# Performance work log

Hardware: AMD Instinct MI355X
Metric: run time of the kernel (lower is better)

## Reference

```python
import jax, jax.numpy as jnp
import numpy as np

NB, NC = 100000, 10000   # buildings, communities
EB, EC = 400000, 80000   # edges
BD, CD = 64, 32          # feature dims


def _glorot(key, shape):
    fan_in = shape[-2] if len(shape) > 1 else shape[0]
    return jax.random.normal(key, shape, jnp.float32) * (1.0 / np.sqrt(fan_in))


def setup_inputs() -> dict:
    key = jax.random.key(0)
    ks = iter(jax.random.split(key, 40))
    inp = {}
    inp['building_features'] = jax.random.normal(next(ks), (NB, BD), jnp.float32)
    inp['community_features'] = jax.random.normal(next(ks), (NC, CD), jnp.float32)
    inp['building_edge_index'] = jax.random.randint(next(ks), (2, EB), 0, NB, jnp.int32)
    inp['community_edge_index'] = jax.random.randint(next(ks), (2, EC), 0, NC, jnp.int32)
    inp['building_to_comm_mapping'] = jax.random.randint(next(ks), (NB,), 0, NC, jnp.int32)
    inp['c1_wl'] = _glorot(next(ks), (CD, 512)); inp['c1_wr'] = _glorot(next(ks), (CD, 512))
    inp['c1_att'] = _glorot(next(ks), (8, 64)); inp['c1_b'] = jnp.zeros((512,), jnp.float32)
    inp['c2_wl'] = _glorot(next(ks), (512, 128)); inp['c2_wr'] = _glorot(next(ks), (512, 128))
    inp['c2_att'] = _glorot(next(ks), (4, 32)); inp['c2_b'] = jnp.zeros((128,), jnp.float32)
    # feature attention: 8 heads of MLP (64+128)->128->2
    inp['fa_w1'] = _glorot(next(ks), (8, BD + 128, 128)); inp['fa_b1'] = jnp.zeros((8, 128), jnp.float32)
    inp['fa_w2'] = _glorot(next(ks), (8, 128, 2)); inp['fa_b2'] = jnp.zeros((8, 2), jnp.float32)
    inp['b1_wl'] = _glorot(next(ks), (BD + 128, 512)); inp['b1_wr'] = _glorot(next(ks), (BD + 128, 512))
    inp['b1_att'] = _glorot(next(ks), (8, 64)); inp['b1_b'] = jnp.zeros((512,), jnp.float32)
    inp['b2_wl'] = _glorot(next(ks), (512, 128)); inp['b2_wr'] = _glorot(next(ks), (512, 128))
    inp['b2_att'] = _glorot(next(ks), (4, 32)); inp['b2_b'] = jnp.zeros((128,), jnp.float32)
    inp['b3_wl'] = _glorot(next(ks), (128, 2)); inp['b3_wr'] = _glorot(next(ks), (128, 2))
    inp['b3_att'] = _glorot(next(ks), (1, 2)); inp['b3_b'] = jnp.zeros((2,), jnp.float32)
    return inp


def gatv2(x, src, dst, wl, wr, att, b, heads, out_dim, concat=True):
    """PyG GATv2Conv (eval mode, self-loops already appended to src/dst)."""
    n = x.shape[0]
    xl = (x @ wl).reshape(n, heads, out_dim)  # source transform
    xr = (x @ wr).reshape(n, heads, out_dim)  # target transform
    e = jax.nn.leaky_relu(xl[src] + xr[dst], 0.2)          # [E,H,D]
    logits = jnp.einsum('ehd,hd->eh', e, att)              # [E,H]
    m = jax.ops.segment_max(logits, dst, num_segments=n)   # stable softmax per target
    p = jnp.exp(logits - m[dst])
    denom = jax.ops.segment_sum(p, dst, num_segments=n)
    alpha = p / denom[dst]
    agg = jax.ops.segment_sum(alpha[:, :, None] * xl[src], dst, num_segments=n)
    agg = agg.reshape(n, heads * out_dim) if concat else agg.mean(axis=1)
    return agg + b


def _with_self_loops(edge_index, n):
    loops = jnp.arange(n, dtype=edge_index.dtype)
    return (jnp.concatenate([edge_index[0], loops]), jnp.concatenate([edge_index[1], loops]))


def _forward(building_features, community_features,
             c1_wl, c1_wr, c1_att, c1_b, c2_wl, c2_wr, c2_att, c2_b,
             fa_w1, fa_b1, fa_w2, fa_b2,
             b1_wl, b1_wr, b1_att, b1_b, b2_wl, b2_wr, b2_att, b2_b,
             b3_wl, b3_wr, b3_att, b3_b,
             building_edge_index, community_edge_index, building_to_comm_mapping):
    csrc, cdst = _with_self_loops(community_edge_index, NC)
    bsrc, bdst = _with_self_loops(building_edge_index, NB)
    # community GNN (dropout is identity in eval)
    cx = jax.nn.relu(gatv2(community_features, csrc, cdst, c1_wl, c1_wr, c1_att, c1_b, 8, 64))
    cx = jax.nn.relu(gatv2(cx, csrc, cdst, c2_wl, c2_wr, c2_att, c2_b, 4, 32))  # [NC,128]
    bcf = cx[building_to_comm_mapping]                                          # [NB,128]
    # multi-head feature attention fusion (vectorized over 8 heads)
    combined = jnp.concatenate([building_features, bcf], axis=1)                # [NB,192]
    h = jax.nn.relu(jnp.einsum('nf,hfk->nhk', combined, fa_w1) + fa_b1)         # [NB,8,128]
    w = jax.nn.softmax(jnp.einsum('nhk,hko->nho', h, fa_w2) + fa_b2, axis=-1)   # [NB,8,2]
    wmean = w.mean(axis=1)                                                      # mean over heads == mean of weighted copies
    fused = jnp.concatenate([building_features * wmean[:, 0:1], bcf * wmean[:, 1:2]], axis=1)
    # building GNN (single batched graph == Batch.from_data_list over all communities)
    x = jax.nn.relu(gatv2(fused, bsrc, bdst, b1_wl, b1_wr, b1_att, b1_b, 8, 64))
    x = jax.nn.relu(gatv2(x, bsrc, bdst, b2_wl, b2_wr, b2_att, b2_b, 4, 32))
    x = gatv2(x, bsrc, bdst, b3_wl, b3_wr, b3_att, b3_b, 1, 2)                   # [NB,2]
    return jax.nn.log_softmax(x, axis=1)


def reference(building_features, community_features,
              c1_wl, c1_wr, c1_att, c1_b, c2_wl, c2_wr, c2_att, c2_b,
              fa_w1, fa_b1, fa_w2, fa_b2,
              b1_wl, b1_wr, b1_att, b1_b, b2_wl, b2_wr, b2_att, b2_b,
              b3_wl, b3_wr, b3_att, b3_b,
              building_edge_index, community_edge_index, building_to_comm_mapping):
    return _forward(building_features, community_features,
                    c1_wl, c1_wr, c1_att, c1_b, c2_wl, c2_wr, c2_att, c2_b,
                    fa_w1, fa_b1, fa_w2, fa_b2,
                    b1_wl, b1_wr, b1_att, b1_b, b2_wl, b2_wr, b2_att, b2_b,
                    b3_wl, b3_wr, b3_att, b3_b,
                    building_edge_index, community_edge_index, building_to_comm_mapping)
```

## Files before the change

kernel.cpp:

```cpp
#include <hip/hip_runtime.h>

static constexpr int NBLD = 100000, NCOM = 10000, EBU = 400000, ECO = 80000;
static constexpr int EBT = EBU + NBLD;
static constexpr int ECT = ECO + NCOM;

typedef _Float16 f16;
typedef _Float16 f16x2 __attribute__((ext_vector_type(2)));
typedef _Float16 f16x8 __attribute__((ext_vector_type(8)));
typedef float f32x4 __attribute__((ext_vector_type(4)));

static constexpr size_t OFF_X1H  = 0;
static constexpr size_t OFF_CXL  = 0;
static constexpr size_t OFF_CXR  = 10240000;
static constexpr size_t OFF_CX1  = 20480000;
static constexpr size_t OFF_CX2L = 30720000;
static constexpr size_t OFF_CX2R = 33280000;
static constexpr size_t OFF_X2   = 0;
static constexpr size_t OFF_XLH  = 102400000;
static constexpr size_t OFF_XRH  = 128000000;
static constexpr size_t OFF_XL2  = 102400000;
static constexpr size_t OFF_XR2  = 128000000;
static constexpr size_t OFF_BF16 = 153600000;
static constexpr size_t OFF_CXF16= 166400000;
static constexpr size_t OFF_WM   = 168960000;
static constexpr size_t OFF_XL3  = 169760000;
static constexpr size_t OFF_XR3  = 170560000;
static constexpr size_t OFF_FAW  = 171360000;
static constexpr size_t OFF_B1LT = 171753216;
static constexpr size_t OFF_B1RT = 171949824;
static constexpr size_t OFF_B2T  = 172146432;
static constexpr size_t OFF_BOFF = 172408576;
static constexpr size_t OFF_BCUR = 172808592;
static constexpr size_t OFF_BSRC = 173208592;
static constexpr size_t OFF_COFF = 175208592;
static constexpr size_t OFF_CCUR = 175248608;
static constexpr size_t OFF_CSRC = 175288608;
static constexpr size_t OFF_SC1  = 175648608;
static constexpr size_t OFF_SC2  = 175649632;
static constexpr size_t OFF_SC1C = 175650656;
static constexpr size_t OFF_SC2C = 175651680;
static constexpr size_t OFF_C1T  = 175700000;
static constexpr size_t OFF_C2T  = 175765536;
static constexpr size_t OFF_CF16 = 176027680;

static constexpr int LP = 40;

__global__ void k_zerof(float* __restrict__ p, int n) {
  int i = blockIdx.x * blockDim.x + threadIdx.x;
  if (i < n) p[i] = 0.f;
}

__global__ void k_cvt4(const float* __restrict__ a, f16* __restrict__ b, int n4) {
  int i = blockIdx.x * blockDim.x + threadIdx.x;
  if (i >= n4) return;
  float4 f = *(const float4*)(a + (size_t)i * 4);
  f16x2 h0; h0[0] = (f16)f.x; h0[1] = (f16)f.y;
  f16x2 h1; h1[0] = (f16)f.z; h1[1] = (f16)f.w;
  *(unsigned*)(b + (size_t)i * 4)     = __builtin_bit_cast(unsigned, h0);
  *(unsigned*)(b + (size_t)i * 4 + 2) = __builtin_bit_cast(unsigned, h1);
}

__global__ void k_cvtall(const float* __restrict__ fa_w1,
                         const float* __restrict__ b1_wl, const float* __restrict__ b1_wr,
                         const float* __restrict__ b2_wl, const float* __restrict__ b2_wr,
                         const float* __restrict__ c1_wl, const float* __restrict__ c1_wr,
                         const float* __restrict__ c2_wl, const float* __restrict__ c2_wr,
                         f16* __restrict__ FAW, f16* __restrict__ B1LT, f16* __restrict__ B1RT,
                         f16* __restrict__ B2T, f16* __restrict__ C1T, f16* __restrict__ C2T) {
  int seg = blockIdx.y;
  const float* W; f16* T; int K, N;
  if (seg < 8)        { W = fa_w1 + (size_t)seg * 192 * 128; T = FAW + (size_t)seg * 128 * 192; K = 192; N = 128; }
  else if (seg == 8)  { W = b1_wl; T = B1LT; K = 192; N = 512; }
  else if (seg == 9)  { W = b1_wr; T = B1RT; K = 192; N = 512; }
  else if (seg == 10) { W = b2_wl; T = B2T;  K = 512; N = 128; }
  else if (seg == 11) { W = b2_wr; T = B2T + 128 * 512; K = 512; N = 128; }
  else if (seg == 12) { W = c1_wl; T = C1T;  K = 32;  N = 512; }
  else if (seg == 13) { W = c1_wr; T = C1T + 512 * 32; K = 32; N = 512; }
  else if (seg == 14) { W = c2_wl; T = C2T;  K = 512; N = 128; }
  else                { W = c2_wr; T = C2T + 128 * 512; K = 512; N = 128; }
  int i = blockIdx.x * blockDim.x + threadIdx.x;
  if (i >= K * N) return;
  int n = i / K, k = i - n * K;
  T[(size_t)n * K + k] = (f16)W[(size_t)k * N + n];
}

__global__ void k_zero2(int* __restrict__ a, int na, int* __restrict__ b, int nb) {
  int i = blockIdx.x * blockDim.x + threadIdx.x;
  if (i < na) a[i] = 0;
  else if (i - na < nb) b[i - na] = 0;
}

__global__ void k_count2(const int* __restrict__ bdst, const int* __restrict__ cdst,
                         int* __restrict__ bcnt, int* __restrict__ ccnt) {
  int e = blockIdx.x * blockDim.x + threadIdx.x;
  if (e < EBT) {
    int dst = (e < EBU) ? bdst[e] : (e - EBU);
    atomicAdd(&bcnt[dst], 1);
  } else {
    int e2 = e - EBT;
    if (e2 >= ECT) return;
    int dst = (e2 < ECO) ? cdst[e2] : (e2 - ECO);
    atomicAdd(&ccnt[dst], 1);
  }
}

__global__ void k_scan1g(const int* __restrict__ bcnt, const int* __restrict__ ccnt,
                         int* __restrict__ boff, int* __restrict__ coff,
                         int* __restrict__ bsum, int* __restrict__ csum) {
  const int* cnt = blockIdx.y ? ccnt : bcnt;
  int* off = blockIdx.y ? coff : boff;
  int* sum = blockIdx.y ? csum : bsum;
  int N = blockIdx.y ? NCOM : NBLD;
  __shared__ int sh[256];
  int tid = threadIdx.x;
  int base = blockIdx.x * 2048 + tid * 8;
  int c[8]; int s = 0;
#pragma unroll
  for (int j = 0; j < 8; ++j) { int i = base + j; c[j] = (i < N) ? cnt[i] : 0; s += c[j]; }
  sh[tid] = s; __syncthreads();
  int own = s;
  for (int o = 1; o < 256; o <<= 1) {
    int v = (tid >= o) ? sh[tid - o] : 0; __syncthreads();
    sh[tid] += v; __syncthreads();
  }
  int ex = sh[tid] - own;
#pragma unroll
  for (int j = 0; j < 8; ++j) { int i = base + j; if (i < N) off[i] = ex; ex += c[j]; }
  if (tid == 255) sum[blockIdx.x] = sh[255];
}

__global__ void k_scan2g(const int* __restrict__ bsum, const int* __restrict__ csum,
                         int nb, int nc, int* __restrict__ bpre, int* __restrict__ cpre) {
  const int* sum = blockIdx.x ? csum : bsum;
  int n = blockIdx.x ? nc : nb;
  int* pre = blockIdx.x ? cpre : bpre;
  __shared__ int sh[256];
  int tid = threadIdx.x;
  int v0 = (tid < n) ? sum[tid] : 0;
  sh[tid] = v0; __syncthreads();
  for (int o = 1; o < 256; o <<= 1) {
    int v = (tid >= o) ? sh[tid - o] : 0; __syncthreads();
    sh[tid] += v; __syncthreads();
  }
  pre[tid] = sh[tid] - v0;
}

__global__ void k_scan3c(int* __restrict__ off, int N, const int* __restrict__ bpre, int Et,
                         int* __restrict__ cur) {
  int i = blockIdx.x * blockDim.x + threadIdx.x;
  if (i < N) {
    int v = off[i] + bpre[i >> 11];
    off[i] = v;
    cur[i] = v;
  }
  if (i == 0) off[N] = Et;
}

__global__ void k_scatter2(const int* __restrict__ bsrc, const int* __restrict__ bdst,
                           const int* __restrict__ csrc, const int* __restrict__ cdst,
                           int* __restrict__ bcur, int* __restrict__ ccur,
                           int* __restrict__ bout, int* __restrict__ cout) {
  int e = blockIdx.x * blockDim.x + threadIdx.x;
  if (e < EBT) {
    int s, d;
    if (e < EBU) { s = bsrc[e]; d = bdst[e]; } else { s = d = e - EBU; }
    bout[atomicAdd(&bcur[d], 1)] = s;
  } else {
    int e2 = e - EBT;
    if (e2 >= ECT) return;
    int s, d;
    if (e2 < ECO) { s = csrc[e2]; d = cdst[e2]; } else { s = d = e2 - ECO; }
    cout[atomicAdd(&ccur[d], 1)] = s;
  }
}


struct frag32 { f16x8 v0, v1; };

static __device__ inline frag32 loadA_lin(const f16* __restrict__ X, int lda,
                                          int k0, int tid, int bm, int M) {
  int row = tid >> 1, half = tid & 1;
  int grow = bm + row;
  frag32 r; r.v0 = (f16x8){}; r.v1 = (f16x8){};
  if (grow < M) {
    const f16* p = X + (size_t)grow * lda + k0 + half * 16;
    r.v0 = *(const f16x8*)(p);
    r.v1 = *(const f16x8*)(p + 8);
  }
  return r;
}

template<bool SCALE>
static __device__ inline frag32 loadA_fused(const f16* __restrict__ bf16h,
                                            const f16* __restrict__ cx16, int mrow,
                                            f16 s0, f16 s1, int k0, int tid, int grow, int M) {
  int half = tid & 1;
  int gc = k0 + half * 16;
  frag32 r; r.v0 = (f16x8){}; r.v1 = (f16x8){};
  if (grow < M) {
    const f16* src; f16 s;
    if (gc < 64) { src = bf16h + (size_t)grow * 64 + gc; s = s0; }
    else         { src = cx16 + (size_t)mrow * 128 + (gc - 64); s = s1; }
    r.v0 = *(const f16x8*)(src);
    r.v1 = *(const f16x8*)(src + 8);
    if (SCALE) {
#pragma unroll
      for (int j = 0; j < 8; ++j) { r.v0[j] *= s; r.v1[j] *= s; }
    }
  }
  return r;
}

static __device__ inline frag32 loadB_T(const f16* __restrict__ WT, int ldk, int k0, int tid) {
  int col = tid >> 1, half = tid & 1;
  const f16* p = WT + (size_t)col * ldk + k0 + half * 16;
  frag32 r;
  r.v0 = *(const f16x8*)(p);
  r.v1 = *(const f16x8*)(p + 8);
  return r;
}

static __device__ inline frag32 loadB_Tpair(const f16* __restrict__ WLt, const f16* __restrict__ WRt,
                                            int ldk, int slab, int k0, int tid) {
  int col = tid >> 1, half = tid & 1;
  const f16* base = (col < 64) ? (WLt + (size_t)(slab + col) * ldk)
                               : (WRt + (size_t)(slab + col - 64) * ldk);
  const f16* p = base + k0 + half * 16;
  frag32 r;
  r.v0 = *(const f16x8*)(p);
  r.v1 = *(const f16x8*)(p + 8);
  return r;
}

static __device__ inline void writeFrag(f16 (*S)[LP], frag32 f, int tid) {
  int row = tid >> 1, half = tid & 1;
  *(f16x8*)&S[row][half * 16]     = f.v0;
  *(f16x8*)&S[row][half * 16 + 8] = f.v1;
}

static __device__ inline void mma_tiles(const f16 (*As)[LP], const f16 (*Bs)[LP],
                                        f32x4 acc[4][4], int wm, int wn, int lane) {
  int rl = lane & 15;
  int kg = (lane >> 4) * 8;
  f16x8 a[4], b[4];
#pragma unroll
  for (int i = 0; i < 4; ++i) a[i] = *(const f16x8*)&As[wm * 64 + i * 16 + rl][kg];
#pragma unroll
  for (int j = 0; j < 4; ++j) b[j] = *(const f16x8*)&Bs[wn * 64 + j * 16 + rl][kg];
#pragma unroll
  for (int i = 0; i < 4; ++i)
#pragma unroll
    for (int j = 0; j < 4; ++j)
      acc[i][j] = __builtin_amdgcn_mfma_f32_16x16x32_f16(a[i], b[j], acc[i][j], 0, 0, 0);
}

template<int NCB>
__global__ __launch_bounds__(256) void k_mgemm_gen(
    const f16* __restrict__ A, int lda,
    const f16* __restrict__ WT, int K,
    f16* __restrict__ out0, f16* __restrict__ out1, int N0, int ldo, int M) {
  __shared__ f16 As[2][128][LP];
  __shared__ f16 Bs[2][128][LP];
  int tid = threadIdx.x;
  int ppx = gridDim.x / (8 * NCB);
  int xcd = blockIdx.x & 7;
  int j6 = blockIdx.x >> 3;
  int cb = j6 % NCB;
  int p = xcd * ppx + j6 / NCB;
  int bm = p * 128;
  if (bm >= M) return;
  int bn = cb * 128;
  int lane = tid & 63, w = tid >> 6, wm_ = w >> 1, wn = w & 1;
  f32x4 acc[4][4];
#pragma unroll
  for (int i = 0; i < 4; ++i)
#pragma unroll
    for (int j = 0; j < 4; ++j) acc[i][j] = (f32x4){0.f, 0.f, 0.f, 0.f};

  const f16* WTb = WT + (size_t)bn * K;
  int NT = K >> 5;
  frag32 a0 = loadA_lin(A, lda, 0, tid, bm, M);
  frag32 b0 = loadB_T(WTb, K, 0, tid);
  frag32 a1; a1.v0 = (f16x8){}; a1.v1 = (f16x8){};
  frag32 b1v = a1;
  if (NT > 1) { a1 = loadA_lin(A, lda, 32, tid, bm, M); b1v = loadB_T(WTb, K, 32, tid); }
  for (int t = 0; t < NT; t += 2) {
    writeFrag(As[0], a0, tid); writeFrag(Bs[0], b0, tid);
    bool two = (t + 1 < NT);
    if (two) { writeFrag(As[1], a1, tid); writeFrag(Bs[1], b1v, tid); }
    __syncthreads();
    if (t + 2 < NT) {
      a0 = loadA_lin(A, lda, (t + 2) * 32, tid, bm, M);
      b0 = loadB_T(WTb, K, (t + 2) * 32, tid);
      if (t + 3 < NT) {
        a1 = loadA_lin(A, lda, (t + 3) * 32, tid, bm, M);
        b1v = loadB_T(WTb, K, (t + 3) * 32, tid);
      }
    }
    mma_tiles(As[0], Bs[0], acc, wm_, wn, lane);
    if (two) mma_tiles(As[1], Bs[1], acc, wm_, wn, lane);
    __syncthreads();
  }
  int rbase = bm + wm_ * 64 + (lane >> 4) * 4;
  int cl = lane & 15;
#pragma unroll
  for (int mi = 0; mi < 4; ++mi)
#pragma unroll
    for (int ni = 0; ni < 4; ++ni) {
      int col = bn + wn * 64 + ni * 16 + cl;
      f16* o; int c;
      if (col < N0) { o = out0; c = col; } else { o = out1; c = col - N0; }
#pragma unroll
      for (int r = 0; r < 4; ++r) {
        int row = rbase + mi * 16 + r;
        if (row < M) o[(size_t)row * ldo + c] = (f16)acc[mi][ni][r];
      }
    }
}

__global__ __launch_bounds__(256) void k_mgemm_b1(
    const f16* __restrict__ bf16h, const f16* __restrict__ cx16,
    const int* __restrict__ map, const float* __restrict__ wmv,
    const f16* __restrict__ WLt, const f16* __restrict__ WRt, int slabBase,
    f16* __restrict__ outl, f16* __restrict__ outr, int M) {
  __shared__ f16 As[2][128][LP];
  __shared__ f16 Bs[2][128][LP];
  int tid = threadIdx.x;
  int ppx = gridDim.x >> 4;
  int xcd = blockIdx.x & 7;
  int j6 = blockIdx.x >> 3;
  int ch = j6 & 1;
  int p = xcd * ppx + (j6 >> 1);
  int bm = p * 128;
  if (bm >= M) return;
  int slab = slabBase + ch * 64;
  int colbase = ch * 64;
  int lane = tid & 63, w = tid >> 6, wm_ = w >> 1, wn = w & 1;
  f32x4 acc[4][4];
#pragma unroll
  for (int i = 0; i < 4; ++i)
#pragma unroll
    for (int j = 0; j < 4; ++j) acc[i][j] = (f32x4){0.f, 0.f, 0.f, 0.f};

  int arow = bm + (tid >> 1);
  int mrow = 0; f16 s0 = (f16)1.f, s1 = (f16)1.f;
  if (arow < M) {
    mrow = map[arow];
    s0 = (f16)wmv[(size_t)arow * 2];
    s1 = (f16)wmv[(size_t)arow * 2 + 1];
  }

  frag32 a0 = loadA_fused<true>(bf16h, cx16, mrow, s0, s1, 0, tid, arow, M);
  frag32 b0 = loadB_Tpair(WLt, WRt, 192, slab, 0, tid);
  frag32 a1 = loadA_fused<true>(bf16h, cx16, mrow, s0, s1, 32, tid, arow, M);
  frag32 b1v = loadB_Tpair(WLt, WRt, 192, slab, 32, tid);
  for (int t = 0; t < 6; t += 2) {
    writeFrag(As[0], a0, tid); writeFrag(Bs[0], b0, tid);
    writeFrag(As[1], a1, tid); writeFrag(Bs[1], b1v, tid);
    __syncthreads();
    if (t + 2 < 6) {
      a0 = loadA_fused<true>(bf16h, cx16, mrow, s0, s1, (t + 2) * 32, tid, arow, M);
      b0 = loadB_Tpair(WLt, WRt, 192, slab, (t + 2) * 32, tid);
      a1 = loadA_fused<true>(bf16h, cx16, mrow, s0, s1, (t + 3) * 32, tid, arow, M);
      b1v = loadB_Tpair(WLt, WRt, 192, slab, (t + 3) * 32, tid);
    }
    mma_tiles(As[0], Bs[0], acc, wm_, wn, lane);
    mma_tiles(As[1], Bs[1], acc, wm_, wn, lane);
    __syncthreads();
  }
  int rbase = bm + wm_ * 64 + (lane >> 4) * 4;
  int cl = lane & 15;
#pragma unroll
  for (int mi = 0; mi < 4; ++mi)
#pragma unroll
    for (int ni = 0; ni < 4; ++ni) {
      int col = wn * 64 + ni * 16 + cl;
      f16* o = (col < 64) ? outl : outr;
      int c = colbase + (col & 63);
#pragma unroll
      for (int r = 0; r < 4; ++r) {
        int row = rbase + mi * 16 + r;
        if (row < M) o[(size_t)row * 128 + c] = (f16)acc[mi][ni][r];
      }
    }
}

__global__ __launch_bounds__(256) void k_mgemm_fa(
    const f16* __restrict__ bf16h, const f16* __restrict__ cx16,
    const int* __restrict__ map,
    const f16* __restrict__ w1T, const float* __restrict__ b1,
    const float* __restrict__ w2, const float* __restrict__ b2,
    float* __restrict__ wmout, int M) {
  __shared__ f16 As[2][128][LP];
  __shared__ f16 Bs[2][128][LP];
  __shared__ float sred[128][4];
  int tid = threadIdx.x;
  int ppx = gridDim.x >> 6;
  int xcd = blockIdx.x & 7;
  int j6 = blockIdx.x >> 3;
  int p = xcd * ppx + (j6 >> 3);
  int h = j6 & 7;
  int bm = p * 128;
  if (bm >= M) return;
  int lane = tid & 63, w = tid >> 6, wm_ = w >> 1, wn = w & 1;
  f32x4 acc[4][4];
#pragma unroll
  for (int i = 0; i < 4; ++i)
#pragma unroll
    for (int j = 0; j < 4; ++j) acc[i][j] = (f32x4){0.f, 0.f, 0.f, 0.f};

  int arow = bm + (tid >> 1);
  int mrow = (arow < M) ? map[arow] : 0;
  const f16* WT = w1T + (size_t)h * 128 * 192;

  frag32 a0 = loadA_fused<false>(bf16h, cx16, mrow, (f16)1.f, (f16)1.f, 0, tid, arow, M);
  frag32 b0 = loadB_T(WT, 192, 0, tid);
  frag32 a1 = loadA_fused<false>(bf16h, cx16, mrow, (f16)1.f, (f16)1.f, 32, tid, arow, M);
  frag32 b1v = loadB_T(WT, 192, 32, tid);
  for (int t = 0; t < 6; t += 2) {
    writeFrag(As[0], a0, tid); writeFrag(Bs[0], b0, tid);
    writeFrag(As[1], a1, tid); writeFrag(Bs[1], b1v, tid);
    __syncthreads();
    if (t + 2 < 6) {
      a0 = loadA_fused<false>(bf16h, cx16, mrow, (f16)1.f, (f16)1.f, (t + 2) * 32, tid, arow, M);
      b0 = loadB_T(WT, 192, (t + 2) * 32, tid);
      a1 = loadA_fused<false>(bf16h, cx16, mrow, (f16)1.f, (f16)1.f, (t + 3) * 32, tid, arow, M);
      b1v = loadB_T(WT, 192, (t + 3) * 32, tid);
    }
    mma_tiles(As[0], Bs[0], acc, wm_, wn, lane);
    mma_tiles(As[1], Bs[1], acc, wm_, wn, lane);
    __syncthreads();
  }

  int cl = lane & 15;
#pragma unroll
  for (int mi = 0; mi < 4; ++mi) {
    float t0[4] = {0.f, 0.f, 0.f, 0.f}, t1[4] = {0.f, 0.f, 0.f, 0.f};
#pragma unroll
    for (int ni = 0; ni < 4; ++ni) {
      int col = wn * 64 + ni * 16 + cl;
      float b1c = b1[h * 128 + col];
      float w0c = w2[((size_t)h * 128 + col) * 2];
      float w1c = w2[((size_t)h * 128 + col) * 2 + 1];
#pragma unroll
      for (int r = 0; r < 4; ++r) {
        float hv = fmaxf(acc[mi][ni][r] + b1c, 0.f);
        t0[r] = fmaf(hv, w0c, t0[r]);
        t1[r] = fmaf(hv, w1c, t1[r]);
      }
    }
#pragma unroll
    for (int m = 1; m < 16; m <<= 1) {
#pragma unroll
      for (int r = 0; r < 4; ++r) { t0[r] += __shfl_xor(t0[r], m); t1[r] += __shfl_xor(t1[r], m); }
    }
    if (cl == 0) {
#pragma unroll
      for (int r = 0; r < 4; ++r) {
        int rib = wm_ * 64 + mi * 16 + (lane >> 4) * 4 + r;
        sred[rib][wn] = t0[r];
        sred[rib][2 + wn] = t1[r];
      }
    }
  }
  __syncthreads();
  if (tid < 128) {
    int grow = bm + tid;
    if (grow < M) {
      float l0 = sred[tid][0] + sred[tid][1] + b2[h * 2];
      float l1 = sred[tid][2] + sred[tid][3] + b2[h * 2 + 1];
      float mx = fmaxf(l0, l1);
      float e0 = __expf(l0 - mx), e1 = __expf(l1 - mx);
      float inv = 0.125f / (e0 + e1);
      atomicAdd(&wmout[(size_t)grow * 2], e0 * inv);
      atomicAdd(&wmout[(size_t)grow * 2 + 1], e1 * inv);
    }
  }
}

template<int V, int G, bool RELU, typename IT, typename OT>
__global__ __launch_bounds__(256) void k_convf(const IT* __restrict__ xl, const IT* __restrict__ xr,
                                               const float* __restrict__ attw, const float* __restrict__ bias,
                                               const int* __restrict__ off, const int* __restrict__ srcl,
                                               OT* __restrict__ outp, int N, int ldx, int ldo) {
  int n = (int)((blockIdx.x * (unsigned)blockDim.x + threadIdx.x) >> 6);
  if (n >= N) return;
  int lane = threadIdx.x & 63;
  int base = lane * V;
  float xr_r[V], att_r[V], acc[V];
#pragma unroll
  for (int j = 0; j < V; ++j) {
    xr_r[j] = (float)xr[(size_t)n * ldx + base + j];
    att_r[j] = attw[base + j];
    acc[j] = 0.f;
  }
  float mh = -INFINITY, lh = 0.f;
  int p0 = off[n], p1 = off[n + 1];

  f16 rawn[V];
  auto ldrow = [&](int src, f16* dst) {
    if constexpr (V == 2 && sizeof(IT) == 2) {
      *(f16x2*)dst = *(const f16x2*)(&xl[(size_t)src * ldx + base]);
    } else if constexpr (V == 8 && sizeof(IT) == 2) {
      *(f16x8*)dst = *(const f16x8*)(&xl[(size_t)src * ldx + base]);
    } else {
#pragma unroll
      for (int j = 0; j < V; ++j) dst[j] = (f16)xl[(size_t)src * ldx + base + j];
    }
  };
  if (p0 < p1) ldrow(srcl[p0], rawn);
  for (int p = p0; p < p1; ++p) {
    f16 raw[V];
#pragma unroll
    for (int j = 0; j < V; ++j) raw[j] = rawn[j];
    if (p + 1 < p1) ldrow(srcl[p + 1], rawn);
    float xlv[V];
#pragma unroll
    for (int j = 0; j < V; ++j) xlv[j] = (float)raw[j];
    float part = 0.f;
#pragma unroll
    for (int j = 0; j < V; ++j) {
      float t = xlv[j] + xr_r[j];
      t = t > 0.f ? t : 0.2f * t;
      part = fmaf(t, att_r[j], part);
    }
#pragma unroll
    for (int m = 1; m < G; m <<= 1) part += __shfl_xor(part, m);
    float mn = fmaxf(mh, part);
    float scl = __expf(mh - mn);
    float pe = __expf(part - mn);
    lh = lh * scl + pe;
#pragma unroll
    for (int j = 0; j < V; ++j) acc[j] = acc[j] * scl + pe * xlv[j];
    mh = mn;
  }
  float inv = 1.f / lh;
#pragma unroll
  for (int j = 0; j < V; ++j) {
    float v = fmaf(acc[j], inv, bias[base + j]);
    if (RELU) v = fmaxf(v, 0.f);
    outp[(size_t)n * ldo + base + j] = (OT)v;
  }
}

__global__ __launch_bounds__(256) void k_b3gemm(const float* __restrict__ x2, const float* __restrict__ wl,
                                                const float* __restrict__ wr,
                                                float* __restrict__ xl3, float* __restrict__ xr3, int NB) {
  int n = (int)((blockIdx.x * (unsigned)blockDim.x + threadIdx.x) >> 6);
  if (n >= NB) return;
  int lane = threadIdx.x & 63;
  float2 a = *(const float2*)(x2 + (size_t)n * 128 + lane * 2);
  float4 wlv = *(const float4*)(wl + lane * 4);
  float4 wrv = *(const float4*)(wr + lane * 4);
  float l0 = a.x * wlv.x + a.y * wlv.z;
  float l1 = a.x * wlv.y + a.y * wlv.w;
  float r0 = a.x * wrv.x + a.y * wrv.z;
  float r1 = a.x * wrv.y + a.y * wrv.w;
#pragma unroll
  for (int m = 1; m < 64; m <<= 1) {
    l0 += __shfl_xor(l0, m); l1 += __shfl_xor(l1, m);
    r0 += __shfl_xor(r0, m); r1 += __shfl_xor(r1, m);
  }
  if (lane == 0) {
    xl3[(size_t)n * 2] = l0; xl3[(size_t)n * 2 + 1] = l1;
    xr3[(size_t)n * 2] = r0; xr3[(size_t)n * 2 + 1] = r1;
  }
}

__global__ void k_conv3(const float* __restrict__ xl, const float* __restrict__ xr,
                        const float* __restrict__ att, const float* __restrict__ bias,
                        const int* __restrict__ off, const int* __restrict__ srcl,
                        float* __restrict__ out, int NB) {
  int n = blockIdx.x * blockDim.x + threadIdx.x;
  if (n >= NB) return;
  float a0 = att[0], a1 = att[1];
  float xr0 = xr[(size_t)n * 2], xr1 = xr[(size_t)n * 2 + 1];
  float mh = -INFINITY, lh = 0.f, c0 = 0.f, c1 = 0.f;
  int p0 = off[n], p1 = off[n + 1];
  float2 rawn = make_float2(0.f, 0.f);
  if (p0 < p1) rawn = *(const float2*)(xl + (size_t)srcl[p0] * 2);
  for (int p = p0; p < p1; ++p) {
    float sl0 = rawn.x, sl1 = rawn.y;
    if (p + 1 < p1) rawn = *(const float2*)(xl + (size_t)srcl[p + 1] * 2);
    float t0 = sl0 + xr0; t0 = t0 > 0.f ? t0 : 0.2f * t0;
    float t1 = sl1 + xr1; t1 = t1 > 0.f ? t1 : 0.2f * t1;
    float lg = t0 * a0 + t1 * a1;
    float mn = fmaxf(mh, lg);
    float scl = __expf(mh - mn);
    float pe = __expf(lg - mn);
    lh = lh * scl + pe;
    c0 = c0 * scl + pe * sl0;
    c1 = c1 * scl + pe * sl1;
    mh = mn;
  }
  float inv = 1.f / lh;
  float v0 = c0 * inv + bias[0];
  float v1 = c1 * inv + bias[1];
  float mx = fmaxf(v0, v1);
  float ls = mx + logf(__expf(v0 - mx) + __expf(v1 - mx));
  out[(size_t)n * 2] = v0 - ls;
  out[(size_t)n * 2 + 1] = v1 - ls;
}

static inline int cdiv(int a, int b) { return (a + b - 1) / b; }

extern "C" void kernel_launch(void* const* d_in, const int* in_sizes, int n_in,
                              void* d_out, int out_size, void* d_ws, size_t ws_size,
                              hipStream_t stream) {
  (void)in_sizes; (void)n_in; (void)out_size; (void)ws_size;
  const float* bfeat = (const float*)d_in[0];
  const float* cfeat = (const float*)d_in[1];
  const int* bei = (const int*)d_in[2];
  const int* cei = (const int*)d_in[3];
  const int* b2c = (const int*)d_in[4];
  const float* c1_wl = (const float*)d_in[5];
  const float* c1_wr = (const float*)d_in[6];
  const float* c1_att = (const float*)d_in[7];
  const float* c1_b = (const float*)d_in[8];
  const float* c2_wl = (const float*)d_in[9];
  const float* c2_wr = (const float*)d_in[10];
  const float* c2_att = (const float*)d_in[11];
  const float* c2_b = (const float*)d_in[12];
  const float* fa_w1 = (const float*)d_in[13];
  const float* fa_b1 = (const float*)d_in[14];
  const float* fa_w2 = (const float*)d_in[15];
  const float* fa_b2 = (const float*)d_in[16];
  const float* b1_wl = (const float*)d_in[17];
  const float* b1_wr = (const float*)d_in[18];
  const float* b1_att = (const float*)d_in[19];
  const float* b1_b = (const float*)d_in[20];
  const float* b2_wl = (const float*)d_in[21];
  const float* b2_wr = (const float*)d_in[22];
  const float* b2_att = (const float*)d_in[23];
  const float* b2_b = (const float*)d_in[24];
  const float* b3_wl = (const float*)d_in[25];
  const float* b3_wr = (const float*)d_in[26];
  const float* b3_att = (const float*)d_in[27];
  const float* b3_b = (const float*)d_in[28];
  char* ws = (char*)d_ws;
  float* out = (float*)d_out;

  const int* b_src_arr = bei;
  const int* b_dst_arr = bei + EBU;
  const int* c_src_arr = cei;
  const int* c_dst_arr = cei + ECO;

  f16*   X1H  = (f16*)(ws + OFF_X1H);
  float* X2   = (float*)(ws + OFF_X2);
  f16*   XLH  = (f16*)(ws + OFF_XLH);
  f16*   XRH  = (f16*)(ws + OFF_XRH);
  f16*   XL2  = (f16*)(ws + OFF_XL2);
  f16*   XR2  = (f16*)(ws + OFF_XR2);
  f16*   CXLh = (f16*)(ws + OFF_CXL);
  f16*   CXRh = (f16*)(ws + OFF_CXR);
  f16*   CX1h = (f16*)(ws + OFF_CX1);
  f16*   CX2Lh= (f16*)(ws + OFF_CX2L);
  f16*   CX2Rh= (f16*)(ws + OFF_CX2R);
  f16*   BF16 = (f16*)(ws + OFF_BF16);
  f16*   CXF16= (f16*)(ws + OFF_CXF16);
  float* WM   = (float*)(ws + OFF_WM);
  float* XL3  = (float*)(ws + OFF_XL3);
  float* XR3  = (float*)(ws + OFF_XR3);
  f16*   FAW  = (f16*)(ws + OFF_FAW);
  f16*   B1LT = (f16*)(ws + OFF_B1LT);
  f16*   B1RT = (f16*)(ws + OFF_B1RT);
  f16*   B2T  = (f16*)(ws + OFF_B2T);
  f16*   C1T  = (f16*)(ws + OFF_C1T);
  f16*   C2T  = (f16*)(ws + OFF_C2T);
  f16*   CF16 = (f16*)(ws + OFF_CF16);
  int* BOFF = (int*)(ws + OFF_BOFF);
  int* BCUR = (int*)(ws + OFF_BCUR);
  int* BSRC = (int*)(ws + OFF_BSRC);
  int* COFF = (int*)(ws + OFF_COFF);
  int* CCUR = (int*)(ws + OFF_CCUR);
  int* CSRC = (int*)(ws + OFF_CSRC);
  int* SC1  = (int*)(ws + OFF_SC1);
  int* SC2  = (int*)(ws + OFF_SC2);
  int* SC1C = (int*)(ws + OFF_SC1C);
  int* SC2C = (int*)(ws + OFF_SC2C);

  k_cvtall<<<dim3(cdiv(192 * 512, 256), 16), 256, 0, stream>>>(
      fa_w1, b1_wl, b1_wr, b2_wl, b2_wr, c1_wl, c1_wr, c2_wl, c2_wr,
      FAW, B1LT, B1RT, B2T, C1T, C2T);
  k_cvt4<<<cdiv(NBLD * 16, 256), 256, 0, stream>>>(bfeat, BF16, NBLD * 16);
  k_cvt4<<<cdiv(NCOM * 8, 256), 256, 0, stream>>>(cfeat, CF16, NCOM * 8);

  k_zero2<<<cdiv(NBLD + NCOM, 256), 256, 0, stream>>>(BCUR, NBLD, CCUR, NCOM);
  k_count2<<<cdiv(EBT + ECT, 256), 256, 0, stream>>>(b_dst_arr, c_dst_arr, BCUR, CCUR);
  k_scan1g<<<dim3(cdiv(NBLD, 2048), 2), 256, 0, stream>>>(BCUR, CCUR, BOFF, COFF, SC1, SC1C);
  k_scan2g<<<2, 256, 0, stream>>>(SC1, SC1C, cdiv(NBLD, 2048), cdiv(NCOM, 2048), SC2, SC2C);
  k_scan3c<<<cdiv(NBLD, 256), 256, 0, stream>>>(BOFF, NBLD, SC2, EBT, BCUR);
  k_scan3c<<<cdiv(NCOM, 256), 256, 0, stream>>>(COFF, NCOM, SC2C, ECT, CCUR);
  k_scatter2<<<cdiv(EBT + ECT, 256), 256, 0, stream>>>(
      b_src_arr, b_dst_arr, c_src_arr, c_dst_arr, BCUR, CCUR, BSRC, CSRC);

  {
    int pC = cdiv(cdiv(NCOM, 128), 8);
    k_mgemm_gen<8><<<8 * pC * 8, 256, 0, stream>>>(
        CF16, 32, C1T, 32, CXLh, CXRh, 512, 512, NCOM);
    k_convf<8, 8, true, f16, f16><<<cdiv(NCOM, 4), 256, 0, stream>>>(
        CXLh, CXRh, c1_att, c1_b, COFF, CSRC, CX1h, NCOM, 512, 512);
    k_mgemm_gen<2><<<8 * pC * 2, 256, 0, stream>>>(
        CX1h, 512, C2T, 512, CX2Lh, CX2Rh, 128, 128, NCOM);
    k_convf<2, 16, true, f16, f16><<<cdiv(NCOM, 4), 256, 0, stream>>>(
        CX2Lh, CX2Rh, c2_att, c2_b, COFF, CSRC, CXF16, NCOM, 128, 128);
  }

  k_zerof<<<cdiv(NBLD * 2, 256), 256, 0, stream>>>(WM, NBLD * 2);
  {
    int panels = cdiv(NBLD, 128);
    int ppx = cdiv(panels, 8);
    k_mgemm_fa<<<64 * ppx, 256, 0, stream>>>(
        BF16, CXF16, b2c, FAW, fa_b1, fa_w2, fa_b2, WM, NBLD);
  }

  {
    int pB = cdiv(cdiv(NBLD, 128), 8);
    for (int cp = 0; cp < 4; ++cp) {
      k_mgemm_b1<<<16 * pB, 256, 0, stream>>>(
          BF16, CXF16, b2c, WM, B1LT, B1RT, cp * 128, XLH, XRH, NBLD);
      k_convf<2, 32, true, f16, f16><<<cdiv(NBLD, 4), 256, 0, stream>>>(
          XLH, XRH, b1_att + cp * 128, b1_b + cp * 128, BOFF, BSRC, X1H + cp * 128, NBLD, 128, 512);
    }
    k_mgemm_gen<2><<<8 * pB * 2, 256, 0, stream>>>(
        X1H, 512, B2T, 512, XL2, XR2, 128, 128, NBLD);
  }

  k_convf<2, 16, true, f16, float><<<cdiv(NBLD, 4), 256, 0, stream>>>(
      XL2, XR2, b2_att, b2_b, BOFF, BSRC, X2, NBLD, 128, 128);

  k_b3gemm<<<cdiv(NBLD, 4), 256, 0, stream>>>(X2, b3_wl, b3_wr, XL3, XR3, NBLD);
  k_conv3<<<cdiv(NBLD, 256), 256, 0, stream>>>(XL3, XR3, b3_att, b3_b, BOFF, BSRC, out, NBLD);
}
```

Baseline: 931.3 us.

## Deepen GEMM register prefetch to four stages with one barrier per k-step

The three MFMA GEMM kernels (generic, b1, fa) now keep four k-tiles of A and B in registers instead of two. The main loop handles one k-tile per iteration, ping-ponging between the two LDS buffers, so it needs one __syncthreads per tile instead of two per pair of tiles. The generic GEMM also takes K as a template parameter, so its loop fully unrolls with constant trip counts. The aim is to hide more global-load latency and cut barrier overhead, at the cost of more VGPRs, which may lower occupancy.

Result: no change. 944.7 us (+1.4%).

```diff
diff --git a/kernel.cpp b/kernel.cpp
--- a/kernel.cpp
+++ b/kernel.cpp
@@ -254,11 +254,12 @@
       acc[i][j] = __builtin_amdgcn_mfma_f32_16x16x32_f16(a[i], b[j], acc[i][j], 0, 0, 0);
 }
 
-template<int NCB>
+template<int K, int NCB>
 __global__ __launch_bounds__(256) void k_mgemm_gen(
     const f16* __restrict__ A, int lda,
-    const f16* __restrict__ WT, int K,
+    const f16* __restrict__ WT,
     f16* __restrict__ out0, f16* __restrict__ out1, int N0, int ldo, int M) {
+  constexpr int NT = K >> 5;
   __shared__ f16 As[2][128][LP];
   __shared__ f16 Bs[2][128][LP];
   int tid = threadIdx.x;
@@ -278,29 +279,22 @@
     for (int j = 0; j < 4; ++j) acc[i][j] = (f32x4){0.f, 0.f, 0.f, 0.f};
 
   const f16* WTb = WT + (size_t)bn * K;
-  int NT = K >> 5;
-  frag32 a0 = loadA_lin(A, lda, 0, tid, bm, M);
-  frag32 b0 = loadB_T(WTb, K, 0, tid);
-  frag32 a1; a1.v0 = (f16x8){}; a1.v1 = (f16x8){};
-  frag32 b1v = a1;
-  if (NT > 1) { a1 = loadA_lin(A, lda, 32, tid, bm, M); b1v = loadB_T(WTb, K, 32, tid); }
-  for (int t = 0; t < NT; t += 2) {
-    writeFrag(As[0], a0, tid); writeFrag(Bs[0], b0, tid);
-    bool two = (t + 1 < NT);
-    if (two) { writeFrag(As[1], a1, tid); writeFrag(Bs[1], b1v, tid); }
+  frag32 ra[4], rb[4];
+#pragma unroll
+  for (int t = 0; t < 4; ++t)
+    if (t < NT) { ra[t] = loadA_lin(A, lda, t * 32, tid, bm, M); rb[t] = loadB_T(WTb, K, t * 32, tid); }
+#pragma unroll
+  for (int t = 0; t < NT; ++t) {
+    writeFrag(As[t & 1], ra[t & 3], tid);
+    writeFrag(Bs[t & 1], rb[t & 3], tid);
     __syncthreads();
-    if (t + 2 < NT) {
-      a0 = loadA_lin(A, lda, (t + 2) * 32, tid, bm, M);
-      b0 = loadB_T(WTb, K, (t + 2) * 32, tid);
-      if (t + 3 < NT) {
-        a1 = loadA_lin(A, lda, (t + 3) * 32, tid, bm, M);
-        b1v = loadB_T(WTb, K, (t + 3) * 32, tid);
-      }
-    }
-    mma_tiles(As[0], Bs[0], acc, wm_, wn, lane);
-    if (two) mma_tiles(As[1], Bs[1], acc, wm_, wn, lane);
-    __syncthreads();
-  }
+    if (t + 4 < NT) {
+      ra[t & 3] = loadA_lin(A, lda, (t + 4) * 32, tid, bm, M);
+      rb[t & 3] = loadB_T(WTb, K, (t + 4) * 32, tid);
+    }
+    mma_tiles(As[t & 1], Bs[t & 1], acc, wm_, wn, lane);
+  }
+  __syncthreads();
   int rbase = bm + wm_ * 64 + (lane >> 4) * 4;
   int cl = lane & 15;
 #pragma unroll
@@ -350,24 +344,24 @@
     s1 = (f16)wmv[(size_t)arow * 2 + 1];
   }
 
-  frag32 a0 = loadA_fused<true>(bf16h, cx16, mrow, s0, s1, 0, tid, arow, M);
-  frag32 b0 = loadB_Tpair(WLt, WRt, 192, slab, 0, tid);
-  frag32 a1 = loadA_fused<true>(bf16h, cx16, mrow, s0, s1, 32, tid, arow, M);
-  frag32 b1v = loadB_Tpair(WLt, WRt, 192, slab, 32, tid);
-  for (int t = 0; t < 6; t += 2) {
-    writeFrag(As[0], a0, tid); writeFrag(Bs[0], b0, tid);
-    writeFrag(As[1], a1, tid); writeFrag(Bs[1], b1v, tid);
+  frag32 ra[4], rb[4];
+#pragma unroll
+  for (int t = 0; t < 4; ++t) {
+    ra[t] = loadA_fused<true>(bf16h, cx16, mrow, s0, s1, t * 32, tid, arow, M);
+    rb[t] = loadB_Tpair(WLt, WRt, 192, slab, t * 32, tid);
+  }
+#pragma unroll
+  for (int t = 0; t < 6; ++t) {
+    writeFrag(As[t & 1], ra[t & 3], tid);
+    writeFrag(Bs[t & 1], rb[t & 3], tid);
     __syncthreads();
-    if (t + 2 < 6) {
-      a0 = loadA_fused<true>(bf16h, cx16, mrow, s0, s1, (t + 2) * 32, tid, arow, M);
-      b0 = loadB_Tpair(WLt, WRt, 192, slab, (t + 2) * 32, tid);
-      a1 = loadA_fused<true>(bf16h, cx16, mrow, s0, s1, (t + 3) * 32, tid, arow, M);
-      b1v = loadB_Tpair(WLt, WRt, 192, slab, (t + 3) * 32, tid);
-    }
-    mma_tiles(As[0], Bs[0], acc, wm_, wn, lane);
-    mma_tiles(As[1], Bs[1], acc, wm_, wn, lane);
-    __syncthreads();
-  }
+    if (t + 4 < 6) {
+      ra[t & 3] = loadA_fused<true>(bf16h, cx16, mrow, s0, s1, (t + 4) * 32, tid, arow, M);
+      rb[t & 3] = loadB_Tpair(WLt, WRt, 192, slab, (t + 4) * 32, tid);
+    }
+    mma_tiles(As[t & 1], Bs[t & 1], acc, wm_, wn, lane);
+  }
+  __syncthreads();
   int rbase = bm + wm_ * 64 + (lane >> 4) * 4;
   int cl = lane & 15;
 #pragma unroll
@@ -413,24 +407,24 @@
   int mrow = (arow < M) ? map[arow] : 0;
   const f16* WT = w1T + (size_t)h * 128 * 192;
 
-  frag32 a0 = loadA_fused<false>(bf16h, cx16, mrow, (f16)1.f, (f16)1.f, 0, tid, arow, M);
-  frag32 b0 = loadB_T(WT, 192, 0, tid);
-  frag32 a1 = loadA_fused<false>(bf16h, cx16, mrow, (f16)1.f, (f16)1.f, 32, tid, arow, M);
-  frag32 b1v = loadB_T(WT, 192, 32, tid);
-  for (int t = 0; t < 6; t += 2) {
-    writeFrag(As[0], a0, tid); writeFrag(Bs[0], b0, tid);
-    writeFrag(As[1], a1, tid); writeFrag(Bs[1], b1v, tid);
+  frag32 ra[4], rb[4];
+#pragma unroll
+  for (int t = 0; t < 4; ++t) {
+    ra[t] = loadA_fused<false>(bf16h, cx16, mrow, (f16)1.f, (f16)1.f, t * 32, tid, arow, M);
+    rb[t] = loadB_T(WT, 192, t * 32, tid);
+  }
+#pragma unroll
+  for (int t = 0; t < 6; ++t) {
+    writeFrag(As[t & 1], ra[t & 3], tid);
+    writeFrag(Bs[t & 1], rb[t & 3], tid);
     __syncthreads();
-    if (t + 2 < 6) {
-      a0 = loadA_fused<false>(bf16h, cx16, mrow, (f16)1.f, (f16)1.f, (t + 2) * 32, tid, arow, M);
-      b0 = loadB_T(WT, 192, (t + 2) * 32, tid);
-      a1 = loadA_fused<false>(bf16h, cx16, mrow, (f16)1.f, (f16)1.f, (t + 3) * 32, tid, arow, M);
-      b1v = loadB_T(WT, 192, (t + 3) * 32, tid);
-    }
-    mma_tiles(As[0], Bs[0], acc, wm_, wn, lane);
-    mma_tiles(As[1], Bs[1], acc, wm_, wn, lane);
-    __syncthreads();
-  }
+    if (t + 4 < 6) {
+      ra[t & 3] = loadA_fused<false>(bf16h, cx16, mrow, (f16)1.f, (f16)1.f, (t + 4) * 32, tid, arow, M);
+      rb[t & 3] = loadB_T(WT, 192, (t + 4) * 32, tid);
+    }
+    mma_tiles(As[t & 1], Bs[t & 1], acc, wm_, wn, lane);
+  }
+  __syncthreads();
 
   int cl = lane & 15;
 #pragma unroll
@@ -696,12 +690,12 @@
 
   {
     int pC = cdiv(cdiv(NCOM, 128), 8);
-    k_mgemm_gen<8><<<8 * pC * 8, 256, 0, stream>>>(
-        CF16, 32, C1T, 32, CXLh, CXRh, 512, 512, NCOM);
+    k_mgemm_gen<32, 8><<<8 * pC * 8, 256, 0, stream>>>(
+        CF16, 32, C1T, CXLh, CXRh, 512, 512, NCOM);
     k_convf<8, 8, true, f16, f16><<<cdiv(NCOM, 4), 256, 0, stream>>>(
         CXLh, CXRh, c1_att, c1_b, COFF, CSRC, CX1h, NCOM, 512, 512);
-    k_mgemm_gen<2><<<8 * pC * 2, 256, 0, stream>>>(
-        CX1h, 512, C2T, 512, CX2Lh, CX2Rh, 128, 128, NCOM);
+    k_mgemm_gen<512, 2><<<8 * pC * 2, 256, 0, stream>>>(
+        CX1h, 512, C2T, CX2Lh, CX2Rh, 128, 128, NCOM);
     k_convf<2, 16, true, f16, f16><<<cdiv(NCOM, 4), 256, 0, stream>>>(
         CX2Lh, CX2Rh, c2_att, c2_b, COFF, CSRC, CXF16, NCOM, 128, 128);
   }
@@ -722,8 +716,8 @@
       k_convf<2, 32, true, f16, f16><<<cdiv(NBLD, 4), 256, 0, stream>>>(
           XLH, XRH, b1_att + cp * 128, b1_b + cp * 128, BOFF, BSRC, X1H + cp * 128, NBLD, 128, 512);
     }
-    k_mgemm_gen<2><<<8 * pB * 2, 256, 0, stream>>>(
-        X1H, 512, B2T, 512, XL2, XR2, 128, 128, NBLD);
+    k_mgemm_gen<512, 2><<<8 * pB * 2, 256, 0, stream>>>(
+        X1H, 512, B2T, XL2, XR2, 128, 128, NBLD);
   }
 
   k_convf<2, 16, true, f16, float><<<cdiv(NBLD, 4), 256, 0, stream>>>(
```
